# Performance work log

Measured on AMD Instinct MI355X. Metric: run time of the kernel, lower is better.

The kernel has to match this reference:

```python
import jax, jax.numpy as jnp
import numpy as np

EPSILON = 0.1
NUM_ITERS = 50
D = 256


def setup_inputs() -> dict:
    key = jax.random.key(0)
    ks = jax.random.split(key, 12)
    NA, NT = 8192, 8192
    s = 1.0 / np.sqrt(D)
    return {
        "agent_embeddings": jax.random.normal(ks[0], (NA, D), jnp.float32),
        "task_embeddings": jax.random.normal(ks[1], (NT, D), jnp.float32),
        "Wq": jax.random.normal(ks[2], (D, D), jnp.float32) * s,
        "bq": jax.random.normal(ks[3], (D,), jnp.float32) * 0.01,
        "Wk": jax.random.normal(ks[4], (D, D), jnp.float32) * s,
        "bk": jax.random.normal(ks[5], (D,), jnp.float32) * 0.01,
        "W1": jax.random.normal(ks[6], (D, D // 2), jnp.float32) * s,
        "b1": jax.random.normal(ks[7], (D // 2,), jnp.float32) * 0.01,
        "W2": jax.random.normal(ks[8], (D // 2, 1), jnp.float32) * (1.0 / np.sqrt(D // 2)),
        "b2": jax.random.normal(ks[9], (1,), jnp.float32) * 0.01,
    }


def _ot_forward(agent_embeddings, task_embeddings, Wq, bq, Wk, bk, W1, b1, W2, b2):
    num_tasks = task_embeddings.shape[0]
    q = agent_embeddings @ Wq + bq  # [NA, D]
    k = task_embeddings @ Wk + bk   # [NT, D]
    q_norm = jnp.sum(q * q, axis=1, keepdims=True)          # [NA, 1]
    k_norm = jnp.sum(k * k, axis=1, keepdims=True)          # [NT, 1]
    distances = q_norm + k_norm.T - 2.0 * (q @ k.T)          # [NA, NT]
    C = -distances
    supply_logits = (jax.nn.relu(agent_embeddings @ W1 + b1) @ W2 + b2)[:, 0]
    b = jax.nn.softmax(supply_logits, axis=0)                # [NA]
    a = jnp.ones((num_tasks,), dtype=C.dtype) / num_tasks    # [NT]

    log_b = jnp.log(b + 1e-20)
    log_a = jnp.log(a + 1e-20)
    log_K = -C / EPSILON                                     # [NA, NT]

    def body(_, fg):
        f, g = fg
        f = log_b - jax.nn.logsumexp(log_K + g[None, :], axis=1)
        g = log_a - jax.nn.logsumexp(log_K + f[:, None], axis=0)
        return (f, g)

    f0 = jnp.zeros_like(b)
    g0 = jnp.zeros_like(a)
    f, g = jax.lax.fori_loop(0, NUM_ITERS, body, (f0, g0))

    T = jnp.exp(f[:, None] + log_K + g[None, :])
    T = jnp.maximum(T, 0.0)
    T = T / (jnp.sum(T) + 1e-08)
    return T


def reference(agent_embeddings, task_embeddings, Wq, bq, Wk, bk, W1, b1, W2, b2):
    return _ot_forward(agent_embeddings, task_embeddings, Wq, bq, Wk, bk, W1, b1, W2, b2)
```

## Files before the change

### kernel.cpp

```cpp
#include <hip/hip_runtime.h>
#include <math.h>

#define NR 8192
#define DIM 256
#define NBLK 512
#define CROWS 16
#define RSC 2
#define NSUB 8
#define SCALE2 14.426950408889634f

typedef unsigned short ushort_t;
typedef __attribute__((ext_vector_type(8))) short bfrag;
typedef __attribute__((ext_vector_type(4))) float facc;

__device__ __forceinline__ float fexp2(float x) {
#if __has_builtin(__builtin_amdgcn_exp2f)
    return __builtin_amdgcn_exp2f(x);
#else
    return exp2f(x);
#endif
}
__device__ __forceinline__ float flog2(float x) {
#if __has_builtin(__builtin_amdgcn_logf)
    return __builtin_amdgcn_logf(x);
#else
    return log2f(x);
#endif
}

__device__ __forceinline__ void gl2lds16(const float* gp, float* lp) {
#if __has_builtin(__builtin_amdgcn_global_load_lds)
    __builtin_amdgcn_global_load_lds(
        (const __attribute__((address_space(1))) unsigned int*)gp,
        (__attribute__((address_space(3))) unsigned int*)lp, 16, 0, 0);
#else
    *(float4*)lp = *(const float4*)gp;
#endif
}

__device__ __forceinline__ void wait_vm0()  { asm volatile("s_waitcnt vmcnt(0)" ::: "memory"); }
__device__ __forceinline__ void bar_lgkm()  { asm volatile("s_waitcnt lgkmcnt(0)\ns_barrier" ::: "memory"); }

__device__ __forceinline__ void lse_comb2(float& m, float& s, float mo, float so) {
    float nm = fmaxf(m, mo);
    s = s * fexp2(m - nm) + so * fexp2(mo - nm);
    m = nm;
}

__device__ __forceinline__ void lse_upd4(float& m, float& s,
                                         float v0, float v1, float v2, float v3) {
    float m4 = fmaxf(fmaxf(v0, v1), fmaxf(v2, v3));
    float nm = fmaxf(m, m4);
    float e = fexp2(v0 - nm) + fexp2(v1 - nm) + fexp2(v2 - nm) + fexp2(v3 - nm);
    s = fmaf(s, fexp2(m - nm), e);
    m = nm;
}

__device__ __forceinline__ void lse_upd2(float& m, float& s, float v0, float v1) {
    float m2 = fmaxf(v0, v1);
    float nm = fmaxf(m, m2);
    float e = fexp2(v0 - nm) + fexp2(v1 - nm);
    s = fmaf(s, fexp2(m - nm), e);
    m = nm;
}

__device__ __forceinline__ ushort_t f2bf(float x) {
    unsigned u = __float_as_uint(x);
    u += 0x7FFFu + ((u >> 16) & 1u);
    return (ushort_t)(u >> 16);
}
__device__ __forceinline__ float bf2f(ushort_t b) {
    return __uint_as_float(((unsigned)b) << 16);
}

__global__ void init_zero(float* __restrict__ g) {
    int t = blockIdx.x * 256 + threadIdx.x;
    if (t < NR) g[t] = 0.0f;
}

__global__ __launch_bounds__(256) void gemm_qk(const float* __restrict__ A,
                                               const float* __restrict__ W,
                                               const float* __restrict__ bias,
                                               float* __restrict__ out) {
    __shared__ float As[16][68];
    __shared__ float Ws[16][68];
    const int t  = threadIdx.x;
    const int r0 = blockIdx.x * 64;
    const int c0 = blockIdx.y * 64;
    const int ty = t >> 4, tx = t & 15;
    const int arow = t >> 2;
    const int ak   = (t & 3) * 4;
    const int wrow = t >> 4;
    const int wcol = (t & 15) * 4;
    float acc[4][4] = {};
    for (int k0 = 0; k0 < DIM; k0 += 16) {
        float4 av = *(const float4*)(A + (size_t)(r0 + arow) * DIM + k0 + ak);
        float4 wv = *(const float4*)(W + (size_t)(k0 + wrow) * DIM + c0 + wcol);
        __syncthreads();
        As[ak + 0][arow] = av.x; As[ak + 1][arow] = av.y;
        As[ak + 2][arow] = av.z; As[ak + 3][arow] = av.w;
        *(float4*)&Ws[wrow][wcol] = wv;
        __syncthreads();
#pragma unroll
        for (int kk = 0; kk < 16; ++kk) {
            float4 a = *(const float4*)&As[kk][ty * 4];
            float4 b = *(const float4*)&Ws[kk][tx * 4];
            float aa[4] = {a.x, a.y, a.z, a.w};
            float bb[4] = {b.x, b.y, b.z, b.w};
#pragma unroll
            for (int i = 0; i < 4; ++i)
#pragma unroll
                for (int j = 0; j < 4; ++j)
                    acc[i][j] = fmaf(aa[i], bb[j], acc[i][j]);
        }
    }
#pragma unroll
    for (int i = 0; i < 4; ++i) {
        float4 o;
        o.x = acc[i][0] + bias[c0 + tx * 4 + 0];
        o.y = acc[i][1] + bias[c0 + tx * 4 + 1];
        o.z = acc[i][2] + bias[c0 + tx * 4 + 2];
        o.w = acc[i][3] + bias[c0 + tx * 4 + 3];
        *(float4*)(out + (size_t)(r0 + ty * 4 + i) * DIM + c0 + tx * 4) = o;
    }
}

__global__ __launch_bounds__(64) void row_norm(const float* __restrict__ x,
                                               float* __restrict__ out) {
    const int row = blockIdx.x, lane = threadIdx.x;
    float4 v = *(const float4*)(x + (size_t)row * DIM + lane * 4);
    float s = v.x * v.x + v.y * v.y + v.z * v.z + v.w * v.w;
#pragma unroll
    for (int off = 32; off > 0; off >>= 1) s += __shfl_xor(s, off);
    if (lane == 0) out[row] = s;
}

__global__ __launch_bounds__(256) void split_bf16(const float* __restrict__ x,
                                                  ushort_t* __restrict__ hi,
                                                  ushort_t* __restrict__ lo) {
    const int idx = (blockIdx.x * 256 + threadIdx.x) * 4;
    float4 v = *(const float4*)(x + idx);
    ushort_t h0 = f2bf(v.x), h1 = f2bf(v.y), h2 = f2bf(v.z), h3 = f2bf(v.w);
    ushort4 hv = make_ushort4(h0, h1, h2, h3);
    ushort4 lv = make_ushort4(f2bf(v.x - bf2f(h0)), f2bf(v.y - bf2f(h1)),
                              f2bf(v.z - bf2f(h2)), f2bf(v.w - bf2f(h3)));
    *(ushort4*)(hi + idx) = hv;
    *(ushort4*)(lo + idx) = lv;
}

__global__ __launch_bounds__(256) void dist_mfma(const ushort_t* __restrict__ qh,
                                                 const ushort_t* __restrict__ ql,
                                                 const ushort_t* __restrict__ kh,
                                                 const ushort_t* __restrict__ kl,
                                                 const float* __restrict__ qn,
                                                 const float* __restrict__ kn,
                                                 float* __restrict__ S) {
    const int t = threadIdx.x;
    const int wv = t >> 6, lane = t & 63;
    const int r0 = blockIdx.y * 128 + (wv >> 1) * 64;
    const int c0 = blockIdx.x * 128 + (wv & 1) * 64;
    const int fr = lane & 15;
    const int fq = lane >> 4;
    facc acc[4][4];
#pragma unroll
    for (int i = 0; i < 4; ++i)
#pragma unroll
        for (int j = 0; j < 4; ++j) acc[i][j] = (facc){0.f, 0.f, 0.f, 0.f};

    for (int k0 = 0; k0 < DIM; k0 += 32) {
        const int ks = k0 + fq * 8;
        bfrag ah[4], al[4], bh[4], bl[4];
#pragma unroll
        for (int mi = 0; mi < 4; ++mi) {
            const size_t ao = (size_t)(r0 + mi * 16 + fr) * DIM + ks;
            ah[mi] = *(const bfrag*)(qh + ao);
            al[mi] = *(const bfrag*)(ql + ao);
        }
#pragma unroll
        for (int ni = 0; ni < 4; ++ni) {
            const size_t bo = (size_t)(c0 + ni * 16 + fr) * DIM + ks;
            bh[ni] = *(const bfrag*)(kh + bo);
            bl[ni] = *(const bfrag*)(kl + bo);
        }
#pragma unroll
        for (int mi = 0; mi < 4; ++mi)
#pragma unroll
            for (int ni = 0; ni < 4; ++ni) {
                acc[mi][ni] = __builtin_amdgcn_mfma_f32_16x16x32_bf16(ah[mi], bh[ni], acc[mi][ni], 0, 0, 0);
                acc[mi][ni] = __builtin_amdgcn_mfma_f32_16x16x32_bf16(ah[mi], bl[ni], acc[mi][ni], 0, 0, 0);
                acc[mi][ni] = __builtin_amdgcn_mfma_f32_16x16x32_bf16(al[mi], bh[ni], acc[mi][ni], 0, 0, 0);
                acc[mi][ni] = __builtin_amdgcn_mfma_f32_16x16x32_bf16(al[mi], bl[ni], acc[mi][ni], 0, 0, 0);
            }
    }
#pragma unroll
    for (int mi = 0; mi < 4; ++mi) {
        float qnr[4];
#pragma unroll
        for (int r = 0; r < 4; ++r) qnr[r] = qn[r0 + mi * 16 + fq * 4 + r];
#pragma unroll
        for (int ni = 0; ni < 4; ++ni) {
            const int col = c0 + ni * 16 + fr;
            const float knc = kn[col];
#pragma unroll
            for (int r = 0; r < 4; ++r) {
                const int row = r0 + mi * 16 + fq * 4 + r;
                S[(size_t)row * NR + col] = (qnr[r] + knc - 2.0f * acc[mi][ni][r]) * SCALE2;
            }
        }
    }
}

__global__ __launch_bounds__(128) void mlp_logits(const float* __restrict__ A,
                                                  const float* __restrict__ W1,
                                                  const float* __restrict__ b1,
                                                  const float* __restrict__ W2,
                                                  const float* __restrict__ b2,
                                                  float* __restrict__ logits) {
    __shared__ float ar[DIM];
    __shared__ float red[2];
    const int t = threadIdx.x;
    const int row = blockIdx.x;
    *(float2*)&ar[t * 2] = *(const float2*)(A + (size_t)row * DIM + t * 2);
    __syncthreads();
    float h = b1[t];
#pragma unroll 8
    for (int kk = 0; kk < DIM; ++kk) h = fmaf(ar[kk], W1[kk * 128 + t], h);
    float val = fmaxf(h, 0.0f) * W2[t];
#pragma unroll
    for (int off = 32; off > 0; off >>= 1) val += __shfl_xor(val, off);
    if ((t & 63) == 0) red[t >> 6] = val;
    __syncthreads();
    if (t == 0) logits[row] = red[0] + red[1] + b2[0];
}

__global__ __launch_bounds__(1024) void softmax_logb(const float* __restrict__ logits,
                                                     float* __restrict__ logb2) {
    __shared__ float redm[16], reds[16];
    const int t = threadIdx.x;
    float l[8];
    float m = -INFINITY;
#pragma unroll
    for (int i = 0; i < 8; ++i) { l[i] = logits[i * 1024 + t]; m = fmaxf(m, l[i]); }
#pragma unroll
    for (int off = 32; off > 0; off >>= 1) m = fmaxf(m, __shfl_xor(m, off));
    if ((t & 63) == 0) redm[t >> 6] = m;
    __syncthreads();
    if (t < 64) {
        float v = (t < 16) ? redm[t] : -INFINITY;
#pragma unroll
        for (int off = 8; off > 0; off >>= 1) v = fmaxf(v, __shfl_xor(v, off));
        if (t == 0) redm[0] = v;
    }
    __syncthreads();
    m = redm[0];
    float s = 0.0f;
#pragma unroll
    for (int i = 0; i < 8; ++i) s += __expf(l[i] - m);
#pragma unroll
    for (int off = 32; off > 0; off >>= 1) s += __shfl_xor(s, off);
    if ((t & 63) == 0) reds[t >> 6] = s;
    __syncthreads();
    if (t < 64) {
        float v = (t < 16) ? reds[t] : 0.0f;
#pragma unroll
        for (int off = 8; off > 0; off >>= 1) v += __shfl_xor(v, off);
        if (t == 0) reds[0] = v;
    }
    __syncthreads();
    s = reds[0];
    float invs = 1.0f / s;
#pragma unroll
    for (int i = 0; i < 8; ++i)
        logb2[i * 1024 + t] = log2f(__expf(l[i] - m) * invs + 1e-20f);
}

__global__ __launch_bounds__(512, 4) void iter_fused(const float* __restrict__ S,
                                                     const float* __restrict__ g,
                                                     const float* __restrict__ logb2,
                                                     float* __restrict__ f,
                                                     float* __restrict__ pm) {
    __shared__ float buf[RSC][NR];
    __shared__ float redm[8], reds[8];
    const int t = threadIdx.x;
    const int wv = t >> 6, lane = t & 63;
    const int chunk = blockIdx.x;
    const int r0 = chunk * CROWS;
    const int rw = wv >> 2;
    const int qt = wv & 3;
    const int qbase = qt * 2048;
    const int loff = lane * 4;

    float4 greg[8];
#pragma unroll
    for (int it = 0; it < 8; ++it)
        greg[it] = *(const float4*)(g + qbase + it * 256 + loff);

    float cm[4][4], cs[4][4];
#pragma unroll
    for (int j = 0; j < 4; ++j)
#pragma unroll
        for (int c = 0; c < 4; ++c) { cm[j][c] = -INFINITY; cs[j][c] = 0.0f; }

    {
        const float* Sr = S + (size_t)(r0 + rw) * NR + qbase;
        float* ld = &buf[rw][qbase];
#pragma unroll
        for (int it = 0; it < 8; ++it)
#if __has_builtin(__builtin_amdgcn_global_load_lds)
            gl2lds16(Sr + it * 256 + loff, ld + it * 256);
#else
            gl2lds16(Sr + it * 256 + loff, ld + it * 256 + loff);
#endif
    }

    for (int sc = 0; sc < NSUB; ++sc) {
        wait_vm0();
        float m = -INFINITY, s = 0.0f;
#pragma unroll
        for (int it = 0; it < 8; ++it) {
            float4 v = *(const float4*)&buf[rw][qbase + it * 256 + loff];
            float4 gv = greg[it];
            lse_upd4(m, s, v.x + gv.x, v.y + gv.y, v.z + gv.z, v.w + gv.w);
        }
#pragma unroll
        for (int off = 32; off > 0; off >>= 1) {
            float mo = __shfl_xor(m, off);
            float so = __shfl_xor(s, off);
            lse_comb2(m, s, mo, so);
        }
        if (lane == 0) { redm[wv] = m; reds[wv] = s; }
        bar_lgkm();

        float fr[RSC];
#pragma unroll
        for (int r = 0; r < RSC; ++r) {
            float mm = redm[r * 4 + 0], ss = reds[r * 4 + 0];
            lse_comb2(mm, ss, redm[r * 4 + 1], reds[r * 4 + 1]);
            lse_comb2(mm, ss, redm[r * 4 + 2], reds[r * 4 + 2]);
            lse_comb2(mm, ss, redm[r * 4 + 3], reds[r * 4 + 3]);
            fr[r] = logb2[r0 + sc * RSC + r] - (mm + flog2(ss));
        }
        if (t < RSC) f[r0 + sc * RSC + t] = fr[t];

#pragma unroll
        for (int j = 0; j < 4; ++j) {
            const int c = j * 2048 + t * 4;
            float4 a = *(const float4*)&buf[0][c];
            float4 bb = *(const float4*)&buf[1][c];
            lse_upd2(cm[j][0], cs[j][0], a.x + fr[0], bb.x + fr[1]);
            lse_upd2(cm[j][1], cs[j][1], a.y + fr[0], bb.y + fr[1]);
            lse_upd2(cm[j][2], cs[j][2], a.z + fr[0], bb.z + fr[1]);
            lse_upd2(cm[j][3], cs[j][3], a.w + fr[0], bb.w + fr[1]);
        }
        bar_lgkm();

        if (sc + 1 < NSUB) {
            const float* Sn = S + (size_t)(r0 + (sc + 1) * RSC + rw) * NR + qbase;
            float* ld = &buf[rw][qbase];
#pragma unroll
            for (int it = 0; it < 8; ++it)
#if __has_builtin(__builtin_amdgcn_global_load_lds)
                gl2lds16(Sn + it * 256 + loff, ld + it * 256);
#else
                gl2lds16(Sn + it * 256 + loff, ld + it * 256 + loff);
#endif
        }
    }
#pragma unroll
    for (int j = 0; j < 4; ++j) {
        float4 L;
        L.x = cm[j][0] + flog2(cs[j][0]);
        L.y = cm[j][1] + flog2(cs[j][1]);
        L.z = cm[j][2] + flog2(cs[j][2]);
        L.w = cm[j][3] + flog2(cs[j][3]);
        *(float4*)&pm[(size_t)chunk * NR + j * 2048 + t * 4] = L;
    }
}

__global__ __launch_bounds__(256) void col_combine(const float* __restrict__ pm,
                                                   float* __restrict__ g,
                                                   float log_a2) {
    __shared__ float Lsh[8][32];
    const int cl = threadIdx.x & 31;
    const int gp = threadIdx.x >> 5;
    const int col = blockIdx.x * 32 + cl;
    float m = -INFINITY, s = 0.0f;
#pragma unroll
    for (int ch = gp * 64; ch < gp * 64 + 64; ch += 4) {
        float l0 = pm[(size_t)(ch + 0) * NR + col];
        float l1 = pm[(size_t)(ch + 1) * NR + col];
        float l2 = pm[(size_t)(ch + 2) * NR + col];
        float l3 = pm[(size_t)(ch + 3) * NR + col];
        lse_upd4(m, s, l0, l1, l2, l3);
    }
    Lsh[gp][cl] = m + flog2(s);
    __syncthreads();
    if (gp == 0) {
        float mm = -INFINITY, ss = 0.0f;
        lse_upd4(mm, ss, Lsh[0][cl], Lsh[1][cl], Lsh[2][cl], Lsh[3][cl]);
        lse_upd4(mm, ss, Lsh[4][cl], Lsh[5][cl], Lsh[6][cl], Lsh[7][cl]);
        g[col] = log_a2 - (mm + flog2(ss));
    }
}

__global__ __launch_bounds__(256) void write_pass(const float* S,
                                                  const float* __restrict__ f,
                                                  const float* __restrict__ g,
                                                  float* out) {
    const int wv = threadIdx.x >> 6, lane = threadIdx.x & 63;
    const int row = blockIdx.x * 4 + wv;
    const float fi = f[row];
    const float4* Sr = (const float4*)(S + (size_t)row * NR);
    const float4* gr = (const float4*)g;
    float4* Or = (float4*)(out + (size_t)row * NR);
#pragma unroll 4
    for (int it = 0; it < NR / 256; ++it) {
        const int idx = it * 64 + lane;
        float4 sv = Sr[idx];
        float4 gv = gr[idx];
        float4 o;
        o.x = fexp2(fi + sv.x + gv.x);
        o.y = fexp2(fi + sv.y + gv.y);
        o.z = fexp2(fi + sv.z + gv.z);
        o.w = fexp2(fi + sv.w + gv.w);
        Or[idx] = o;
    }
}

extern "C" void kernel_launch(void* const* d_in, const int* in_sizes, int n_in,
                              void* d_out, int out_size, void* d_ws, size_t ws_size,
                              hipStream_t stream) {
    (void)in_sizes; (void)n_in; (void)out_size; (void)ws_size;
    const float* A  = (const float*)d_in[0];
    const float* Tk = (const float*)d_in[1];
    const float* Wq = (const float*)d_in[2];
    const float* bq = (const float*)d_in[3];
    const float* Wk = (const float*)d_in[4];
    const float* bk = (const float*)d_in[5];
    const float* W1 = (const float*)d_in[6];
    const float* b1 = (const float*)d_in[7];
    const float* W2 = (const float*)d_in[8];
    const float* b2 = (const float*)d_in[9];
    float* S  = (float*)d_out;
    float* ws = (float*)d_ws;
    float* qn     = ws; ws += NR;
    float* kn     = ws; ws += NR;
    float* logb2  = ws; ws += NR;
    float* logits = ws; ws += NR;
    float* f      = ws; ws += NR;
    float* g      = ws; ws += NR;
    float* pm     = ws; ws += (size_t)NBLK * NR;
    float* q      = ws; ws += (size_t)NR * DIM;
    float* k      = ws; ws += (size_t)NR * DIM;
    ushort_t* qh = (ushort_t*)pm;
    ushort_t* ql = qh + (size_t)NR * DIM;
    ushort_t* kh = ql + (size_t)NR * DIM;
    ushort_t* kl = kh + (size_t)NR * DIM;

    const float log_a2 = -13.0f;

    init_zero<<<32, 256, 0, stream>>>(g);
    gemm_qk<<<dim3(128, 4), 256, 0, stream>>>(A, Wq, bq, q);
    gemm_qk<<<dim3(128, 4), 256, 0, stream>>>(Tk, Wk, bk, k);
    row_norm<<<NR, 64, 0, stream>>>(q, qn);
    row_norm<<<NR, 64, 0, stream>>>(k, kn);
    split_bf16<<<NR * DIM / 1024, 256, 0, stream>>>(q, qh, ql);
    split_bf16<<<NR * DIM / 1024, 256, 0, stream>>>(k, kh, kl);
    mlp_logits<<<NR, 128, 0, stream>>>(A, W1, b1, W2, b2, logits);
    softmax_logb<<<1, 1024, 0, stream>>>(logits, logb2);
    dist_mfma<<<dim3(64, 64), 256, 0, stream>>>(qh, ql, kh, kl, qn, kn, S);
    for (int it = 0; it < 50; ++it) {
        iter_fused<<<NBLK, 512, 0, stream>>>(S, g, logb2, f, pm);
        col_combine<<<NR / 32, 256, 0, stream>>>(pm, g, log_a2);
    }
    write_pass<<<NR / 4, 256, 0, stream>>>(S, f, g, S);
}
```

Before: 3.450 ms.

## Double-buffer S rows one at a time so loads overlap compute

```diff
diff --git a/kernel.cpp b/kernel.cpp
--- a/kernel.cpp
+++ b/kernel.cpp
@@ -5,8 +5,7 @@
 #define DIM 256
 #define NBLK 512
 #define CROWS 16
-#define RSC 2
-#define NSUB 8
+#define NSUB 16
 #define SCALE2 14.426950408889634f
 
 typedef unsigned short ushort_t;
@@ -39,6 +38,7 @@
 }
 
 __device__ __forceinline__ void wait_vm0()  { asm volatile("s_waitcnt vmcnt(0)" ::: "memory"); }
+__device__ __forceinline__ void wait_vm4()  { asm volatile("s_waitcnt vmcnt(4)" ::: "memory"); }
 __device__ __forceinline__ void bar_lgkm()  { asm volatile("s_waitcnt lgkmcnt(0)\ns_barrier" ::: "memory"); }
 
 __device__ __forceinline__ void lse_comb2(float& m, float& s, float mo, float so) {
@@ -56,11 +56,9 @@
     m = nm;
 }
 
-__device__ __forceinline__ void lse_upd2(float& m, float& s, float v0, float v1) {
-    float m2 = fmaxf(v0, v1);
-    float nm = fmaxf(m, m2);
-    float e = fexp2(v0 - nm) + fexp2(v1 - nm);
-    s = fmaf(s, fexp2(m - nm), e);
+__device__ __forceinline__ void lse_upd1(float& m, float& s, float v) {
+    float nm = fmaxf(m, v);
+    s = fmaf(s, fexp2(m - nm), fexp2(v - nm));
     m = nm;
 }
 
@@ -279,21 +277,22 @@
                                                      const float* __restrict__ logb2,
                                                      float* __restrict__ f,
                                                      float* __restrict__ pm) {
-    __shared__ float buf[RSC][NR];
+    __shared__ float buf[2][NR];
     __shared__ float redm[8], reds[8];
+    __shared__ float lbsh[CROWS];
     const int t = threadIdx.x;
     const int wv = t >> 6, lane = t & 63;
     const int chunk = blockIdx.x;
     const int r0 = chunk * CROWS;
-    const int rw = wv >> 2;
-    const int qt = wv & 3;
-    const int qbase = qt * 2048;
+    const int seg = wv * 1024;
     const int loff = lane * 4;
 
-    float4 greg[8];
-#pragma unroll
-    for (int it = 0; it < 8; ++it)
-        greg[it] = *(const float4*)(g + qbase + it * 256 + loff);
+    if (t < CROWS) lbsh[t] = logb2[r0 + t];
+
+    float4 greg[4];
+#pragma unroll
+    for (int it = 0; it < 4; ++it)
+        greg[it] = *(const float4*)(g + seg + it * 256 + loff);
 
     float cm[4][4], cs[4][4];
 #pragma unroll
@@ -302,23 +301,33 @@
         for (int c = 0; c < 4; ++c) { cm[j][c] = -INFINITY; cs[j][c] = 0.0f; }
 
     {
-        const float* Sr = S + (size_t)(r0 + rw) * NR + qbase;
-        float* ld = &buf[rw][qbase];
-#pragma unroll
-        for (int it = 0; it < 8; ++it)
+        const float* S0 = S + (size_t)(r0 + 0) * NR + seg;
+        const float* S1 = S + (size_t)(r0 + 1) * NR + seg;
+#pragma unroll
+        for (int it = 0; it < 4; ++it)
 #if __has_builtin(__builtin_amdgcn_global_load_lds)
-            gl2lds16(Sr + it * 256 + loff, ld + it * 256);
-#else
-            gl2lds16(Sr + it * 256 + loff, ld + it * 256 + loff);
-#endif
-    }
-
+            gl2lds16(S0 + it * 256 + loff, &buf[0][seg + it * 256]);
+#else
+            gl2lds16(S0 + it * 256 + loff, &buf[0][seg + it * 256 + loff]);
+#endif
+#pragma unroll
+        for (int it = 0; it < 4; ++it)
+#if __has_builtin(__builtin_amdgcn_global_load_lds)
+            gl2lds16(S1 + it * 256 + loff, &buf[1][seg + it * 256]);
+#else
+            gl2lds16(S1 + it * 256 + loff, &buf[1][seg + it * 256 + loff]);
+#endif
+    }
+
+    float fmine = 0.0f;
     for (int sc = 0; sc < NSUB; ++sc) {
-        wait_vm0();
+        const int p = sc & 1;
+        if (sc < NSUB - 1) wait_vm4(); else wait_vm0();
+
         float m = -INFINITY, s = 0.0f;
 #pragma unroll
-        for (int it = 0; it < 8; ++it) {
-            float4 v = *(const float4*)&buf[rw][qbase + it * 256 + loff];
+        for (int it = 0; it < 4; ++it) {
+            float4 v = *(const float4*)&buf[p][seg + it * 256 + loff];
             float4 gv = greg[it];
             lse_upd4(m, s, v.x + gv.x, v.y + gv.y, v.z + gv.z, v.w + gv.w);
         }
@@ -331,41 +340,44 @@
         if (lane == 0) { redm[wv] = m; reds[wv] = s; }
         bar_lgkm();
 
-        float fr[RSC];
-#pragma unroll
-        for (int r = 0; r < RSC; ++r) {
-            float mm = redm[r * 4 + 0], ss = reds[r * 4 + 0];
-            lse_comb2(mm, ss, redm[r * 4 + 1], reds[r * 4 + 1]);
-            lse_comb2(mm, ss, redm[r * 4 + 2], reds[r * 4 + 2]);
-            lse_comb2(mm, ss, redm[r * 4 + 3], reds[r * 4 + 3]);
-            fr[r] = logb2[r0 + sc * RSC + r] - (mm + flog2(ss));
-        }
-        if (t < RSC) f[r0 + sc * RSC + t] = fr[t];
+        float m0 = redm[0], s0 = reds[0];
+        lse_comb2(m0, s0, redm[1], reds[1]);
+        float m2 = redm[2], s2 = reds[2];
+        lse_comb2(m2, s2, redm[3], reds[3]);
+        float m4 = redm[4], s4 = reds[4];
+        lse_comb2(m4, s4, redm[5], reds[5]);
+        float m6 = redm[6], s6 = reds[6];
+        lse_comb2(m6, s6, redm[7], reds[7]);
+        lse_comb2(m0, s0, m2, s2);
+        lse_comb2(m4, s4, m6, s6);
+        lse_comb2(m0, s0, m4, s4);
+        const float fr = lbsh[sc] - (m0 + flog2(s0));
+        if (t == sc) fmine = fr;
 
 #pragma unroll
         for (int j = 0; j < 4; ++j) {
             const int c = j * 2048 + t * 4;
-            float4 a = *(const float4*)&buf[0][c];
-            float4 bb = *(const float4*)&buf[1][c];
-            lse_upd2(cm[j][0], cs[j][0], a.x + fr[0], bb.x + fr[1]);
-            lse_upd2(cm[j][1], cs[j][1], a.y + fr[0], bb.y + fr[1]);
-            lse_upd2(cm[j][2], cs[j][2], a.z + fr[0], bb.z + fr[1]);
-            lse_upd2(cm[j][3], cs[j][3], a.w + fr[0], bb.w + fr[1]);
+            float4 a = *(const float4*)&buf[p][c];
+            lse_upd1(cm[j][0], cs[j][0], a.x + fr);
+            lse_upd1(cm[j][1], cs[j][1], a.y + fr);
+            lse_upd1(cm[j][2], cs[j][2], a.z + fr);
+            lse_upd1(cm[j][3], cs[j][3], a.w + fr);
         }
         bar_lgkm();
 
-        if (sc + 1 < NSUB) {
-            const float* Sn = S + (size_t)(r0 + (sc + 1) * RSC + rw) * NR + qbase;
-            float* ld = &buf[rw][qbase];
-#pragma unroll
-            for (int it = 0; it < 8; ++it)
+        if (sc + 2 < NSUB) {
+            const float* Sn = S + (size_t)(r0 + sc + 2) * NR + seg;
+#pragma unroll
+            for (int it = 0; it < 4; ++it)
 #if __has_builtin(__builtin_amdgcn_global_load_lds)
-                gl2lds16(Sn + it * 256 + loff, ld + it * 256);
-#else
-                gl2lds16(Sn + it * 256 + loff, ld + it * 256 + loff);
-#endif
-        }
-    }
+                gl2lds16(Sn + it * 256 + loff, &buf[p][seg + it * 256]);
+#else
+                gl2lds16(Sn + it * 256 + loff, &buf[p][seg + it * 256 + loff]);
+#endif
+        }
+    }
+    if (t < CROWS) f[r0 + t] = fmine;
+
 #pragma unroll
     for (int j = 0; j < 4; ++j) {
         float4 L;
```

Measured after the change: 3.947 ms. +14.4%, slower.
